# Optimization experiments

Hardware: AMD Instinct MI355X
Metric: run time of the kernel (lower is better)

## Reference

```python
import jax, jax.numpy as jnp
import numpy as np

BETA = 0.01

def quaternion_to_matrix(q):
    # q: (..., 4) real-part-first, not necessarily normalized
    r, i, j, k = q[..., 0], q[..., 1], q[..., 2], q[..., 3]
    two_s = 2.0 / jnp.sum(q * q, axis=-1)
    o = jnp.stack([
        1 - two_s * (j * j + k * k), two_s * (i * j - k * r), two_s * (i * k + j * r),
        two_s * (i * j + k * r), 1 - two_s * (i * i + k * k), two_s * (j * k - i * r),
        two_s * (i * k - j * r), two_s * (j * k + i * r), 1 - two_s * (i * i + j * j),
    ], axis=-1)
    return o.reshape(q.shape[:-1] + (3, 3))

def smooth_l1(x, target):
    d = jnp.abs(x - target)
    return jnp.where(d < BETA, 0.5 * d * d / BETA, d - 0.5 * BETA)

def setup_inputs() -> dict:
    key = jax.random.key(0)
    ks = jax.random.split(key, 5)
    b = 2097152
    return {
        "point_clouds": jax.random.normal(ks[0], (b, 3), dtype=jnp.float32),
        "target_transl": jax.random.normal(ks[1], (b, 3), dtype=jnp.float32),
        "target_rot": jax.random.normal(ks[2], (b, 4), dtype=jnp.float32),
        "transl_err": jax.random.normal(ks[3], (b, 3), dtype=jnp.float32),
        "rot_err": jax.random.normal(ks[4], (b, 4), dtype=jnp.float32),
    }

def reference(point_clouds, target_transl, target_rot, transl_err, rot_err):
    b = target_transl.shape[0]
    # pose_inverse: per-sample 3x3 inverse (vectorized, replaces the Python loop)
    R = quaternion_to_matrix(target_rot)                       # (b,3,3)
    R_inv = jnp.linalg.inv(R)                                  # (b,3,3)
    T_inv = -jnp.einsum('bij,bj->bi', R_inv, target_transl)    # (b,3)

    pred_r = quaternion_to_matrix(rot_err)                     # (b,3,3)
    pred_t = transl_err                                        # (b,3)

    # rotation loss against identity (flattened)
    r_mul = jnp.einsum('bij,bjk->bik', R_inv, pred_r).reshape(b, 9)
    eye9 = jnp.eye(3, dtype=r_mul.dtype).reshape(1, 9)
    loss_r = jnp.mean(jnp.sum(smooth_l1(r_mul, eye9), axis=1))

    # translation loss against zeros
    t_mul = jnp.einsum('bij,bj->bi', pred_r, T_inv) + pred_t   # (b,3)
    loss_t = jnp.mean(jnp.sum(smooth_l1(t_mul, 0.0), axis=1))

    total_loss = loss_r + loss_t
    return jnp.stack([total_loss, loss_t, loss_r])
```

## Files before the change

### kernel.cpp

```cpp
#include <hip/hip_runtime.h>

#define SL1_BETA 0.01f
#define NSLOT   256
#define CHUNK   512
#define LDS_TQ  0
#define LDS_QE  8192
#define LDS_TT  16384
#define LDS_TE  22528
#define LDS_BYTES 28672

#define AS1(p) ((const __attribute__((address_space(1))) void*)(p))
#define AS3(p) ((__attribute__((address_space(3))) void*)(p))

__device__ __forceinline__ float smooth_l1(float x) {
    float d = fabsf(x);
    return (d < SL1_BETA) ? (0.5f * d * d / SL1_BETA) : (d - 0.5f * SL1_BETA);
}

__device__ __forceinline__ void quat_to_mat9(float4 q, float R[9]) {
    float r = q.x, i = q.y, j = q.z, k = q.w;
    float two_s = 2.0f / (r*r + i*i + j*j + k*k);
    R[0] = 1.0f - two_s * (j*j + k*k);
    R[1] = two_s * (i*j - k*r);
    R[2] = two_s * (i*k + j*r);
    R[3] = two_s * (i*j + k*r);
    R[4] = 1.0f - two_s * (i*i + k*k);
    R[5] = two_s * (j*k - i*r);
    R[6] = two_s * (i*k - j*r);
    R[7] = two_s * (j*k + i*r);
    R[8] = 1.0f - two_s * (i*i + j*j);
}

__device__ __forceinline__ void sample_loss(float4 q, float4 e,
                                            float t0, float t1, float t2,
                                            float p0, float p1, float p2,
                                            float& sr, float& st) {
    float R[9], P[9];
    quat_to_mat9(q, R);
    quat_to_mat9(e, P);

    #pragma unroll
    for (int i2 = 0; i2 < 3; ++i2) {
        #pragma unroll
        for (int j2 = 0; j2 < 3; ++j2) {
            float v = R[0*3 + i2] * P[0*3 + j2]
                    + R[1*3 + i2] * P[1*3 + j2]
                    + R[2*3 + i2] * P[2*3 + j2];
            sr += smooth_l1(v - (i2 == j2 ? 1.0f : 0.0f));
        }
    }

    float Ti0 = -(R[0]*t0 + R[3]*t1 + R[6]*t2);
    float Ti1 = -(R[1]*t0 + R[4]*t1 + R[7]*t2);
    float Ti2 = -(R[2]*t0 + R[5]*t1 + R[8]*t2);

    st += smooth_l1(P[0]*Ti0 + P[1]*Ti1 + P[2]*Ti2 + p0);
    st += smooth_l1(P[3]*Ti0 + P[4]*Ti1 + P[5]*Ti2 + p1);
    st += smooth_l1(P[6]*Ti0 + P[7]*Ti1 + P[8]*Ti2 + p2);
}

__global__ __launch_bounds__(256) void euler_loss_kernel(
        const float*  __restrict__ tt,
        const float4* __restrict__ tq,
        const float*  __restrict__ te,
        const float4* __restrict__ qe,
        double* __restrict__ acc, int b) {
    __shared__ __align__(16) unsigned char smem[LDS_BYTES];
    int t    = threadIdx.x;
    int lane = t & 63;
    int wid  = t >> 6;
    long long base = (long long)blockIdx.x * CHUNK;

    float sr = 0.0f, st = 0.0f;
    bool full = (base + CHUNK <= (long long)b);
    if (full) {
        #pragma unroll
        for (int u = 0; u < 7; ++u) {
            int o = wid * 7 + u;
            const unsigned char* src;
            if (o < 8)       src = (const unsigned char*)tq + base * 16 + (size_t)o        * 1024;
            else if (o < 16) src = (const unsigned char*)qe + base * 16 + (size_t)(o - 8)  * 1024;
            else if (o < 22) src = (const unsigned char*)tt + base * 12 + (size_t)(o - 16) * 1024;
            else             src = (const unsigned char*)te + base * 12 + (size_t)(o - 22) * 1024;
            __builtin_amdgcn_global_load_lds(AS1(src + (size_t)lane * 16),
                                             AS3(&smem[(size_t)o * 1024]),
                                             16, 0, 0);
        }
        __syncthreads();

        const float4* tqL = (const float4*)&smem[LDS_TQ];
        const float4* qeL = (const float4*)&smem[LDS_QE];
        const float*  ttL = (const float*) &smem[LDS_TT];
        const float*  teL = (const float*) &smem[LDS_TE];
        #pragma unroll
        for (int u = 0; u < 2; ++u) {
            int c = t + u * 256;
            sample_loss(tqL[c], qeL[c],
                        ttL[3*c], ttL[3*c+1], ttL[3*c+2],
                        teL[3*c], teL[3*c+1], teL[3*c+2], sr, st);
        }
    } else {
        for (long long s = base + t; s < (long long)b; s += 256) {
            sample_loss(tq[s], qe[s],
                        tt[3*s], tt[3*s+1], tt[3*s+2],
                        te[3*s], te[3*s+1], te[3*s+2], sr, st);
        }
    }

    #pragma unroll
    for (int off = 32; off > 0; off >>= 1) {
        sr += __shfl_down(sr, off);
        st += __shfl_down(st, off);
    }
    if (lane == 0) {
        int slot = (blockIdx.x * 4 + wid) & (NSLOT - 1);
        double* sp = (double*)((unsigned char*)acc + (size_t)slot * 128);
        atomicAdd(&sp[0], (double)sr);
        atomicAdd(&sp[1], (double)st);
    }
}

__global__ __launch_bounds__(256) void euler_loss_finalize(
        const double* __restrict__ acc, float* __restrict__ out, int b) {
    int t = threadIdx.x;
    const double* sp = (const double*)((const unsigned char*)acc + (size_t)t * 128);
    double sr = sp[0], st = sp[1];
    #pragma unroll
    for (int off = 32; off > 0; off >>= 1) {
        sr += __shfl_down(sr, off);
        st += __shfl_down(st, off);
    }
    __shared__ double s_r[4], s_t[4];
    int lane = t & 63, wid = t >> 6;
    if (lane == 0) { s_r[wid] = sr; s_t[wid] = st; }
    __syncthreads();
    if (t == 0) {
        double tr = s_r[0] + s_r[1] + s_r[2] + s_r[3];
        double tts = s_t[0] + s_t[1] + s_t[2] + s_t[3];
        double inv_b = 1.0 / (double)b;
        double lr = tr * inv_b;
        double lt = tts * inv_b;
        out[0] = (float)(lr + lt);
        out[1] = (float)lt;
        out[2] = (float)lr;
    }
}

extern "C" void kernel_launch(void* const* d_in, const int* in_sizes, int n_in,
                              void* d_out, int out_size, void* d_ws, size_t ws_size,
                              hipStream_t stream) {
    const float*  tt = (const float*)d_in[1];
    const float4* tq = (const float4*)d_in[2];
    const float*  te = (const float*)d_in[3];
    const float4* qe = (const float4*)d_in[4];
    float* out = (float*)d_out;
    int b = in_sizes[1] / 3;

    double* acc = (double*)d_ws;
    hipMemsetAsync(acc, 0, (size_t)NSLOT * 128, stream);

    int grid = (b + CHUNK - 1) / CHUNK;
    euler_loss_kernel<<<grid, 256, 0, stream>>>(tt, tq, te, qe, acc, b);
    euler_loss_finalize<<<1, 256, 0, stream>>>(acc, out, b);
}
```

Before: 34.05 us.

## Switch to persistent grid with per-wave LDS staging and no block barrier

Each wavefront now owns a private LDS buffer and loops over 64-sample chunks in a grid-stride loop. It uses direct global-to-LDS loads, then waits with s_waitcnt instead of a block-wide __syncthreads. The grid is capped at 2048 blocks with a launch-bounds occupancy hint. This is meant to remove block barriers and reduce the number of launched blocks. The trade-off is that each wave issues its load and then waits on it fully, with no double-buffering, so memory latency may be exposed per chunk.

```diff
diff --git a/kernel.cpp b/kernel.cpp
--- a/kernel.cpp
+++ b/kernel.cpp
@@ -2,12 +2,10 @@
 
 #define SL1_BETA 0.01f
 #define NSLOT   256
-#define CHUNK   512
-#define LDS_TQ  0
-#define LDS_QE  8192
-#define LDS_TT  16384
-#define LDS_TE  22528
-#define LDS_BYTES 28672
+#define WCHUNK  64
+#define WBUF    3584
+#define NW      4
+#define LDS_BYTES (NW * WBUF)
 
 #define AS1(p) ((const __attribute__((address_space(1))) void*)(p))
 #define AS3(p) ((__attribute__((address_space(3))) void*)(p))
@@ -59,51 +57,61 @@
     st += smooth_l1(P[6]*Ti0 + P[7]*Ti1 + P[8]*Ti2 + p2);
 }
 
-__global__ __launch_bounds__(256) void euler_loss_kernel(
+__global__ __launch_bounds__(256, 8) void euler_loss_kernel(
         const float*  __restrict__ tt,
         const float4* __restrict__ tq,
         const float*  __restrict__ te,
         const float4* __restrict__ qe,
         double* __restrict__ acc, int b) {
     __shared__ __align__(16) unsigned char smem[LDS_BYTES];
-    int t    = threadIdx.x;
-    int lane = t & 63;
-    int wid  = t >> 6;
-    long long base = (long long)blockIdx.x * CHUNK;
+    const int t    = threadIdx.x;
+    const int lane = t & 63;
+    const int wid  = t >> 6;
+    unsigned char* my = smem + (size_t)wid * WBUF;
+
+    const int gw   = blockIdx.x * NW + wid;
+    const int totW = gridDim.x * NW;
+    const long long nch = ((long long)b + WCHUNK - 1) / WCHUNK;
+
+    const float4* tqL = (const float4*)(my);
+    const float4* qeL = (const float4*)(my + 1024);
+    const float*  ttL = (const float*)(my + 2048);
+    const float*  teL = (const float*)(my + 2816);
 
     float sr = 0.0f, st = 0.0f;
-    bool full = (base + CHUNK <= (long long)b);
-    if (full) {
-        #pragma unroll
-        for (int u = 0; u < 7; ++u) {
-            int o = wid * 7 + u;
-            const unsigned char* src;
-            if (o < 8)       src = (const unsigned char*)tq + base * 16 + (size_t)o        * 1024;
-            else if (o < 16) src = (const unsigned char*)qe + base * 16 + (size_t)(o - 8)  * 1024;
-            else if (o < 22) src = (const unsigned char*)tt + base * 12 + (size_t)(o - 16) * 1024;
-            else             src = (const unsigned char*)te + base * 12 + (size_t)(o - 22) * 1024;
-            __builtin_amdgcn_global_load_lds(AS1(src + (size_t)lane * 16),
-                                             AS3(&smem[(size_t)o * 1024]),
-                                             16, 0, 0);
-        }
-        __syncthreads();
+    for (long long c = gw; c < nch; c += totW) {
+        long long s0 = c * WCHUNK;
+        bool full = (s0 + WCHUNK <= (long long)b);
+        if (full) {
+            asm volatile("s_waitcnt lgkmcnt(0)" ::: "memory");
+            __builtin_amdgcn_global_load_lds(
+                AS1((const unsigned char*)tq + s0 * 16 + (size_t)lane * 16),
+                AS3(my), 16, 0, 0);
+            __builtin_amdgcn_global_load_lds(
+                AS1((const unsigned char*)qe + s0 * 16 + (size_t)lane * 16),
+                AS3(my + 1024), 16, 0, 0);
+            if (lane < 48) {
+                __builtin_amdgcn_global_load_lds(
+                    AS1((const unsigned char*)tt + s0 * 12 + (size_t)lane * 16),
+                    AS3(my + 2048), 16, 0, 0);
+                __builtin_amdgcn_global_load_lds(
+                    AS1((const unsigned char*)te + s0 * 12 + (size_t)lane * 16),
+                    AS3(my + 2816), 16, 0, 0);
+            }
+            asm volatile("s_waitcnt vmcnt(0)" ::: "memory");
 
-        const float4* tqL = (const float4*)&smem[LDS_TQ];
-        const float4* qeL = (const float4*)&smem[LDS_QE];
-        const float*  ttL = (const float*) &smem[LDS_TT];
-        const float*  teL = (const float*) &smem[LDS_TE];
-        #pragma unroll
-        for (int u = 0; u < 2; ++u) {
-            int c = t + u * 256;
-            sample_loss(tqL[c], qeL[c],
-                        ttL[3*c], ttL[3*c+1], ttL[3*c+2],
-                        teL[3*c], teL[3*c+1], teL[3*c+2], sr, st);
-        }
-    } else {
-        for (long long s = base + t; s < (long long)b; s += 256) {
-            sample_loss(tq[s], qe[s],
-                        tt[3*s], tt[3*s+1], tt[3*s+2],
-                        te[3*s], te[3*s+1], te[3*s+2], sr, st);
+            float4 q = tqL[lane];
+            float4 e = qeL[lane];
+            sample_loss(q, e,
+                        ttL[3*lane], ttL[3*lane+1], ttL[3*lane+2],
+                        teL[3*lane], teL[3*lane+1], teL[3*lane+2], sr, st);
+        } else {
+            long long s = s0 + lane;
+            if (s < (long long)b) {
+                sample_loss(tq[s], qe[s],
+                            tt[3*s], tt[3*s+1], tt[3*s+2],
+                            te[3*s], te[3*s+1], te[3*s+2], sr, st);
+            }
         }
     }
 
@@ -113,7 +121,7 @@
         st += __shfl_down(st, off);
     }
     if (lane == 0) {
-        int slot = (blockIdx.x * 4 + wid) & (NSLOT - 1);
+        int slot = gw & (NSLOT - 1);
         double* sp = (double*)((unsigned char*)acc + (size_t)slot * 128);
         atomicAdd(&sp[0], (double)sr);
         atomicAdd(&sp[1], (double)st);
@@ -135,7 +143,7 @@
     if (lane == 0) { s_r[wid] = sr; s_t[wid] = st; }
     __syncthreads();
     if (t == 0) {
-        double tr = s_r[0] + s_r[1] + s_r[2] + s_r[3];
+        double tr  = s_r[0] + s_r[1] + s_r[2] + s_r[3];
         double tts = s_t[0] + s_t[1] + s_t[2] + s_t[3];
         double inv_b = 1.0 / (double)b;
         double lr = tr * inv_b;
@@ -159,7 +167,10 @@
     double* acc = (double*)d_ws;
     hipMemsetAsync(acc, 0, (size_t)NSLOT * 128, stream);
 
-    int grid = (b + CHUNK - 1) / CHUNK;
+    int grid = 2048;
+    long long nch = ((long long)b + WCHUNK - 1) / WCHUNK;
+    long long maxg = (nch + NW - 1) / NW;
+    if ((long long)grid > maxg) grid = (int)maxg;
     euler_loss_kernel<<<grid, 256, 0, stream>>>(tt, tq, te, qe, acc, b);
     euler_loss_finalize<<<1, 256, 0, stream>>>(acc, out, b);
 }
```

Result: slower. 48.84 us (+43.5%).

## Double-buffer LDS staging in a persistent grid-stride kernel

Applied to the files above, without the earlier changes.

Replaces the one-chunk-per-block kernel with a persistent grid of 1280 blocks. Each block loops over 256-sample chunks and prefetches the next chunk into a second LDS buffer with async global_load_lds while it computes the current one. Per-wave vmcnt waits and raw s_barrier calls control the overlap. The aim is to hide load latency behind compute and cut block launch overhead, at the cost of fragile hand-counted waitcnt values and the risk of too few waves in flight.

```diff
diff --git a/kernel.cpp b/kernel.cpp
--- a/kernel.cpp
+++ b/kernel.cpp
@@ -1,13 +1,10 @@
 #include <hip/hip_runtime.h>
 
 #define SL1_BETA 0.01f
-#define NSLOT   256
-#define CHUNK   512
-#define LDS_TQ  0
-#define LDS_QE  8192
-#define LDS_TT  16384
-#define LDS_TE  22528
-#define LDS_BYTES 28672
+#define NSLOT 256
+#define CHUNK 256
+#define BUFB  14336
+#define LDS_BYTES (2 * BUFB)
 
 #define AS1(p) ((const __attribute__((address_space(1))) void*)(p))
 #define AS3(p) ((__attribute__((address_space(3))) void*)(p))
@@ -59,52 +56,86 @@
     st += smooth_l1(P[6]*Ti0 + P[7]*Ti1 + P[8]*Ti2 + p2);
 }
 
-__global__ __launch_bounds__(256) void euler_loss_kernel(
+__device__ __forceinline__ void stage_ops(
+        const unsigned char* tq8, const unsigned char* qe8,
+        const unsigned char* tt8, const unsigned char* te8,
+        unsigned char* bufbase, long long s0, int wid, int lane) {
+    #pragma unroll
+    for (int u = 0; u < 4; ++u) {
+        int o = wid + 4 * u;
+        if (o < 14) {
+            const unsigned char* src;
+            if (o < 4)       src = tq8 + s0 * 16 + (size_t)o        * 1024;
+            else if (o < 8)  src = qe8 + s0 * 16 + (size_t)(o - 4)  * 1024;
+            else if (o < 11) src = tt8 + s0 * 12 + (size_t)(o - 8)  * 1024;
+            else             src = te8 + s0 * 12 + (size_t)(o - 11) * 1024;
+            __builtin_amdgcn_global_load_lds(AS1(src + (size_t)lane * 16),
+                                             AS3(bufbase + (size_t)o * 1024),
+                                             16, 0, 0);
+        }
+    }
+}
+
+__global__ __launch_bounds__(256, 5) void euler_loss_kernel(
         const float*  __restrict__ tt,
         const float4* __restrict__ tq,
         const float*  __restrict__ te,
         const float4* __restrict__ qe,
         double* __restrict__ acc, int b) {
     __shared__ __align__(16) unsigned char smem[LDS_BYTES];
-    int t    = threadIdx.x;
-    int lane = t & 63;
-    int wid  = t >> 6;
-    long long base = (long long)blockIdx.x * CHUNK;
+    const int t    = threadIdx.x;
+    const int lane = t & 63;
+    const int wid  = t >> 6;
+
+    const unsigned char* tq8 = (const unsigned char*)tq;
+    const unsigned char* qe8 = (const unsigned char*)qe;
+    const unsigned char* tt8 = (const unsigned char*)tt;
+    const unsigned char* te8 = (const unsigned char*)te;
 
     float sr = 0.0f, st = 0.0f;
-    bool full = (base + CHUNK <= (long long)b);
-    if (full) {
-        #pragma unroll
-        for (int u = 0; u < 7; ++u) {
-            int o = wid * 7 + u;
-            const unsigned char* src;
-            if (o < 8)       src = (const unsigned char*)tq + base * 16 + (size_t)o        * 1024;
-            else if (o < 16) src = (const unsigned char*)qe + base * 16 + (size_t)(o - 8)  * 1024;
-            else if (o < 22) src = (const unsigned char*)tt + base * 12 + (size_t)(o - 16) * 1024;
-            else             src = (const unsigned char*)te + base * 12 + (size_t)(o - 22) * 1024;
-            __builtin_amdgcn_global_load_lds(AS1(src + (size_t)lane * 16),
-                                             AS3(&smem[(size_t)o * 1024]),
-                                             16, 0, 0);
+
+    long long nfull = (long long)b / CHUNK;
+    long long c     = blockIdx.x;
+    long long step  = gridDim.x;
+    int cur = 0;
+    bool have = (c < nfull);
+    if (have) stage_ops(tq8, qe8, tt8, te8, smem, c * CHUNK, wid, lane);
+
+    while (have) {
+        long long cn = c + step;
+        bool nhave = (cn < nfull);
+        if (nhave)
+            stage_ops(tq8, qe8, tt8, te8, smem + (cur ^ 1) * BUFB,
+                      cn * CHUNK, wid, lane);
+        if (nhave) {
+            if (wid < 2) { asm volatile("s_waitcnt vmcnt(4)" ::: "memory"); }
+            else         { asm volatile("s_waitcnt vmcnt(3)" ::: "memory"); }
+        } else {
+            asm volatile("s_waitcnt vmcnt(0)" ::: "memory");
         }
-        __syncthreads();
+        __builtin_amdgcn_sched_barrier(0);
+        __builtin_amdgcn_s_barrier();
 
-        const float4* tqL = (const float4*)&smem[LDS_TQ];
-        const float4* qeL = (const float4*)&smem[LDS_QE];
-        const float*  ttL = (const float*) &smem[LDS_TT];
-        const float*  teL = (const float*) &smem[LDS_TE];
-        #pragma unroll
-        for (int u = 0; u < 2; ++u) {
-            int c = t + u * 256;
-            sample_loss(tqL[c], qeL[c],
-                        ttL[3*c], ttL[3*c+1], ttL[3*c+2],
-                        teL[3*c], teL[3*c+1], teL[3*c+2], sr, st);
-        }
-    } else {
-        for (long long s = base + t; s < (long long)b; s += 256) {
-            sample_loss(tq[s], qe[s],
-                        tt[3*s], tt[3*s+1], tt[3*s+2],
-                        te[3*s], te[3*s+1], te[3*s+2], sr, st);
-        }
+        const unsigned char* bp = smem + cur * BUFB;
+        const float4* tqL = (const float4*)(bp);
+        const float4* qeL = (const float4*)(bp + 4096);
+        const float*  ttL = (const float*) (bp + 8192);
+        const float*  teL = (const float*) (bp + 11264);
+        sample_loss(tqL[t], qeL[t],
+                    ttL[3*t], ttL[3*t+1], ttL[3*t+2],
+                    teL[3*t], teL[3*t+1], teL[3*t+2], sr, st);
+
+        __builtin_amdgcn_s_barrier();
+        cur ^= 1;
+        c = cn;
+        have = nhave;
+    }
+
+    for (long long s = nfull * CHUNK + (long long)blockIdx.x * blockDim.x + t;
+         s < (long long)b; s += (long long)gridDim.x * blockDim.x) {
+        sample_loss(tq[s], qe[s],
+                    tt[3*s], tt[3*s+1], tt[3*s+2],
+                    te[3*s], te[3*s+1], te[3*s+2], sr, st);
     }
 
     #pragma unroll
@@ -135,7 +166,7 @@
     if (lane == 0) { s_r[wid] = sr; s_t[wid] = st; }
     __syncthreads();
     if (t == 0) {
-        double tr = s_r[0] + s_r[1] + s_r[2] + s_r[3];
+        double tr  = s_r[0] + s_r[1] + s_r[2] + s_r[3];
         double tts = s_t[0] + s_t[1] + s_t[2] + s_t[3];
         double inv_b = 1.0 / (double)b;
         double lr = tr * inv_b;
@@ -159,7 +190,10 @@
     double* acc = (double*)d_ws;
     hipMemsetAsync(acc, 0, (size_t)NSLOT * 128, stream);
 
-    int grid = (b + CHUNK - 1) / CHUNK;
+    long long nfull = (long long)b / CHUNK;
+    int grid = 1280;
+    if ((long long)grid > nfull) grid = (int)nfull;
+    if (grid < 1) grid = 1;
     euler_loss_kernel<<<grid, 256, 0, stream>>>(tt, tq, te, qe, acc, b);
     euler_loss_finalize<<<1, 256, 0, stream>>>(acc, out, b);
 }
```

Result: slower. 35.41 us (+4.0%).
